# Optimization experiments

Measured on AMD Instinct MI355X. Metric: run time of the kernel, lower is better.

Reference implementation:

```python
import jax, jax.numpy as jnp
import numpy as np

N, L, V, H = 64, 2048, 32000, 512

def setup_inputs() -> dict:
    key = jax.random.key(0)
    ks = jax.random.split(key, 6)
    s = 1.0 / np.sqrt(H)
    return {
        "X": jax.random.randint(ks[0], (N, L), 0, V),
        "emb": jax.random.normal(ks[1], (V, H), jnp.float32),
        "W_hh": jax.random.normal(ks[2], (H, H), jnp.float32) * s,
        "b_hh": jax.random.normal(ks[3], (H,), jnp.float32) * s,
        "W_xh": jax.random.normal(ks[4], (H, H), jnp.float32) * s,
        "b_xh": jax.random.normal(ks[5], (H,), jnp.float32) * s,
    }

def reference(X, emb, W_hh, b_hh, W_xh, b_xh):
    # Embed all timesteps and apply the input projection once (batched GEMM);
    # identical math to per-step W_xh(E_t) + b_xh.
    E = emb[X]                                   # (N, L, H)
    Xh = jnp.einsum('nlh,kh->nlk', E, W_xh) + b_xh  # (N, L, H)

    def step(h, xh_t):
        # h_t = tanh(W_hh h_{t-1} + b_hh + W_xh x_t + b_xh)
        h = jnp.tanh(h @ W_hh.T + b_hh + xh_t)
        return h, h

    h0 = jnp.zeros((X.shape[0], W_hh.shape[0]), dtype=emb.dtype)
    _, H_all = jax.lax.scan(step, h0, jnp.swapaxes(Xh, 0, 1))  # (L, N, H)
    return jnp.swapaxes(H_all, 0, 1)             # (N, L, H)
```

## Files before the change

### kernel.cpp

```cpp
#include <hip/hip_runtime.h>


typedef _Float16 half8 __attribute__((ext_vector_type(8)));
typedef float    f32x4 __attribute__((ext_vector_type(4)));

#define MFMA_F16(A,B,C) __builtin_amdgcn_mfma_f32_16x16x32_f16(A,B,C,0,0,0)

static __device__ __forceinline__ half8 cvt8(const float* p){
  const f32x4* q = (const f32x4*)p;
  f32x4 a = q[0], b = q[1];
  half8 r;
  r[0]=(_Float16)a[0]; r[1]=(_Float16)a[1]; r[2]=(_Float16)a[2]; r[3]=(_Float16)a[3];
  r[4]=(_Float16)b[0]; r[5]=(_Float16)b[1]; r[6]=(_Float16)b[2]; r[7]=(_Float16)b[3];
  return r;
}

static __device__ __forceinline__ float tanh_fast(float z){
  float e = __expf(2.0f*z);
  return 1.0f - 2.0f/(e + 1.0f);
}

__global__ __launch_bounds__(256) void k_xh(
    const int* __restrict__ X, const float* __restrict__ emb,
    const float* __restrict__ Wxh, const float* __restrict__ bxh,
    const float* __restrict__ bhh, float* __restrict__ out)
{
  const int bid = blockIdx.x;
  const int bm = bid >> 3;
  const int bn = bid & 7;
  const int tid = threadIdx.x;
  const int w  = tid >> 6;
  const int l  = tid & 63;
  const int lr = l & 15, lq = l >> 4;

  const int mbase = bm*64 + (w>>1)*32;
  const int nbase = bn*64 + (w&1)*32;

  const int tok0 = X[mbase + lr];
  const int tok1 = X[mbase + 16 + lr];
  const int c0 = nbase + lr;
  const int c1 = nbase + 16 + lr;
  const float bs0 = bxh[c0] + bhh[c0];
  const float bs1 = bxh[c1] + bhh[c1];

  const float* a0 = emb + (long long)tok0*512 + lq*8;
  const float* a1 = emb + (long long)tok1*512 + lq*8;
  const float* b0 = Wxh + (long long)c0*512 + lq*8;
  const float* b1 = Wxh + (long long)c1*512 + lq*8;

  f32x4 acc00 = {0,0,0,0}, acc01 = {0,0,0,0}, acc10 = {0,0,0,0}, acc11 = {0,0,0,0};

  #pragma unroll
  for (int ks=0; ks<16; ++ks){
    half8 A0 = cvt8(a0 + ks*32);
    half8 A1 = cvt8(a1 + ks*32);
    half8 B0 = cvt8(b0 + ks*32);
    half8 B1 = cvt8(b1 + ks*32);
    acc00 = MFMA_F16(A0, B0, acc00);
    acc01 = MFMA_F16(A0, B1, acc01);
    acc10 = MFMA_F16(A1, B0, acc10);
    acc11 = MFMA_F16(A1, B1, acc11);
  }
  #pragma unroll
  for (int r=0; r<4; ++r){
    const long long m0 = mbase + 4*lq + r;
    const long long m1 = m0 + 16;
    out[m0*512 + c0] = acc00[r] + bs0;
    out[m0*512 + c1] = acc01[r] + bs1;
    out[m1*512 + c0] = acc10[r] + bs0;
    out[m1*512 + c1] = acc11[r] + bs1;
  }
}

__global__ __launch_bounds__(512, 2) void k_rnn(
    const float* __restrict__ Whh,
    float* __restrict__ out)
{
  const int b   = blockIdx.x;
  const int tid = threadIdx.x;
  const int w   = tid >> 6;
  const int l   = tid & 63;
  const int lr  = l & 15;
  const int kg  = l >> 4;
  const int wc0 = w * 64;

  __shared__ _Float16 wlds[8][16][512];
  __shared__ _Float16 hbuf[2][2][520];

  for (int i = tid; i < 2*2*520; i += 512) (&hbuf[0][0][0])[i] = (_Float16)0.0f;

  half8 Wv[3][16];
  #pragma unroll
  for (int ct = 0; ct < 3; ++ct){
    #pragma unroll
    for (int ks = 0; ks < 16; ++ks){
      Wv[ct][ks] = cvt8(Whh + (long long)(wc0 + ct*16 + lr)*512 + ks*32 + kg*8);
    }
  }
  #pragma unroll
  for (int ks = 0; ks < 16; ++ks){
    half8 v = cvt8(Whh + (long long)(wc0 + 48 + lr)*512 + ks*32 + kg*8);
    *(half8*)&wlds[w][ks][l*8] = v;
  }
  __syncthreads();

  const int jj = l & 1;
  const long long nb = (long long)(b*2 + (lr < 2 ? lr : 0)) * 2048 * 512;

  for (int t = 0; t < 2048; ++t){
    const int bufc = t & 1, bufp = bufc ^ 1;

    f32x4 xh0 = {0,0,0,0}, xh1 = {0,0,0,0}, xh2 = {0,0,0,0}, xh3 = {0,0,0,0};
    long long ob = 0;
    const bool act = (lr < 2);
    if (act){
      ob = nb + (long long)t*512 + wc0 + kg*4;
      xh0 = *(const f32x4*)(out + ob);
      xh1 = *(const f32x4*)(out + ob + 16);
      xh2 = *(const f32x4*)(out + ob + 32);
      xh3 = *(const f32x4*)(out + ob + 48);
    }

    f32x4 acc0 = {0,0,0,0}, acc1 = {0,0,0,0}, acc2 = {0,0,0,0}, acc3 = {0,0,0,0};

    #pragma unroll
    for (int ks = 0; ks < 16; ++ks){
      half8 hf = *(const half8*)&hbuf[bufp][jj][ks*32 + kg*8];
      half8 w3 = *(const half8*)&wlds[w][ks][l*8];
      acc0 = MFMA_F16(Wv[0][ks], hf, acc0);
      acc1 = MFMA_F16(Wv[1][ks], hf, acc1);
      acc2 = MFMA_F16(Wv[2][ks], hf, acc2);
      acc3 = MFMA_F16(w3, hf, acc3);
    }

    if (act){
      f32x4 h0, h1, h2, h3;
      #pragma unroll
      for (int r = 0; r < 4; ++r){
        h0[r] = tanh_fast(acc0[r] + xh0[r]);
        h1[r] = tanh_fast(acc1[r] + xh1[r]);
        h2[r] = tanh_fast(acc2[r] + xh2[r]);
        h3[r] = tanh_fast(acc3[r] + xh3[r]);
      }
      *(f32x4*)(out + ob)      = h0;
      *(f32x4*)(out + ob + 16) = h1;
      *(f32x4*)(out + ob + 32) = h2;
      *(f32x4*)(out + ob + 48) = h3;

      union { _Float16 h[4]; unsigned long long u; } p0, p1, p2, p3;
      #pragma unroll
      for (int r = 0; r < 4; ++r){
        p0.h[r] = (_Float16)h0[r]; p1.h[r] = (_Float16)h1[r];
        p2.h[r] = (_Float16)h2[r]; p3.h[r] = (_Float16)h3[r];
      }
      const int cl = wc0 + kg*4;
      *(unsigned long long*)&hbuf[bufc][lr][cl]      = p0.u;
      *(unsigned long long*)&hbuf[bufc][lr][cl + 16] = p1.u;
      *(unsigned long long*)&hbuf[bufc][lr][cl + 32] = p2.u;
      *(unsigned long long*)&hbuf[bufc][lr][cl + 48] = p3.u;
    }

    __syncthreads();
  }
}

extern "C" void kernel_launch(void* const* d_in, const int* in_sizes, int n_in,
                              void* d_out, int out_size, void* d_ws, size_t ws_size,
                              hipStream_t stream)
{
  const int*   X    = (const int*)  d_in[0];
  const float* emb  = (const float*)d_in[1];
  const float* Whh  = (const float*)d_in[2];
  const float* bhh  = (const float*)d_in[3];
  const float* Wxh  = (const float*)d_in[4];
  const float* bxh  = (const float*)d_in[5];
  float* out = (float*)d_out;

  hipLaunchKernelGGL(k_xh,  dim3(16384), dim3(256), 0, stream, X, emb, Wxh, bxh, bhh, out);
  hipLaunchKernelGGL(k_rnn, dim3(32),    dim3(512), 0, stream, Whh, out);
}
```

Before: 8.702 ms.

## Batch 16 sequences per RNN block with 4 waves and swizzled LDS hidden state

The recurrent kernel changes from 32 blocks of 8 waves, each handling 2 sequences padded into a 16-wide MFMA tile, to 4 blocks of 4 waves, each handling 16 sequences. That fills the MFMA N dimension instead of wasting most of it on padding. Each wave now owns 128 output columns, with W_hh split between registers (3/4) and LDS (1/4). The hidden state sits in a single XOR-swizzled LDS buffer guarded by two barriers per step instead of double buffering. The trade-off is only 4 CUs in use, more serial MFMA work per wave per timestep, and an extra barrier on the serial chain.

```diff
diff --git a/kernel.cpp b/kernel.cpp
--- a/kernel.cpp
+++ b/kernel.cpp
@@ -72,94 +72,85 @@
   }
 }
 
-__global__ __launch_bounds__(512, 2) void k_rnn(
+__global__ __launch_bounds__(256, 1) void k_rnn(
     const float* __restrict__ Whh,
     float* __restrict__ out)
 {
-  const int b   = blockIdx.x;
+  const int g   = blockIdx.x;
   const int tid = threadIdx.x;
   const int w   = tid >> 6;
   const int l   = tid & 63;
   const int lr  = l & 15;
   const int kg  = l >> 4;
-  const int wc0 = w * 64;
+  const int r7  = lr & 7;
+  const int colbase = w * 128;
 
-  __shared__ _Float16 wlds[8][16][512];
-  __shared__ _Float16 hbuf[2][2][520];
+  __shared__ _Float16 wlds[4][32][512];
+  __shared__ _Float16 hb[16][512];
 
-  for (int i = tid; i < 2*2*520; i += 512) (&hbuf[0][0][0])[i] = (_Float16)0.0f;
+  {
+    f32x4 z = {0,0,0,0};
+    f32x4* hz = (f32x4*)&hb[0][0];
+    for (int i = tid; i < 16*512*2/16; i += 256) hz[i] = z;
+  }
 
-  half8 Wv[3][16];
+  half8 Wreg[8][12];
   #pragma unroll
-  for (int ct = 0; ct < 3; ++ct){
+  for (int ct = 0; ct < 8; ++ct){
+    const float* wp = Whh + (long long)(colbase + ct*16 + lr)*512 + kg*8;
     #pragma unroll
     for (int ks = 0; ks < 16; ++ks){
-      Wv[ct][ks] = cvt8(Whh + (long long)(wc0 + ct*16 + lr)*512 + ks*32 + kg*8);
+      half8 v = cvt8(wp + ks*32);
+      if ((ks & 3) == 0) *(half8*)&wlds[w][ct*4 + (ks>>2)][l*8] = v;
+      else               Wreg[ct][ks - (ks>>2) - 1] = v;
     }
-  }
-  #pragma unroll
-  for (int ks = 0; ks < 16; ++ks){
-    half8 v = cvt8(Whh + (long long)(wc0 + 48 + lr)*512 + ks*32 + kg*8);
-    *(half8*)&wlds[w][ks][l*8] = v;
   }
   __syncthreads();
 
-  const int jj = l & 1;
-  const long long nb = (long long)(b*2 + (lr < 2 ? lr : 0)) * 2048 * 512;
+  const long long nbase = (long long)(g*16 + lr) * (2048LL*512);
 
   for (int t = 0; t < 2048; ++t){
-    const int bufc = t & 1, bufp = bufc ^ 1;
+    const float* op = out + nbase + (long long)t*512 + colbase + kg*4;
+    f32x4 xh[8];
+    #pragma unroll
+    for (int ct = 0; ct < 8; ++ct) xh[ct] = *(const f32x4*)(op + ct*16);
 
-    f32x4 xh0 = {0,0,0,0}, xh1 = {0,0,0,0}, xh2 = {0,0,0,0}, xh3 = {0,0,0,0};
-    long long ob = 0;
-    const bool act = (lr < 2);
-    if (act){
-      ob = nb + (long long)t*512 + wc0 + kg*4;
-      xh0 = *(const f32x4*)(out + ob);
-      xh1 = *(const f32x4*)(out + ob + 16);
-      xh2 = *(const f32x4*)(out + ob + 32);
-      xh3 = *(const f32x4*)(out + ob + 48);
-    }
-
-    f32x4 acc0 = {0,0,0,0}, acc1 = {0,0,0,0}, acc2 = {0,0,0,0}, acc3 = {0,0,0,0};
+    f32x4 acc[8];
+    #pragma unroll
+    for (int ct = 0; ct < 8; ++ct) acc[ct] = (f32x4){0,0,0,0};
 
     #pragma unroll
     for (int ks = 0; ks < 16; ++ks){
-      half8 hf = *(const half8*)&hbuf[bufp][jj][ks*32 + kg*8];
-      half8 w3 = *(const half8*)&wlds[w][ks][l*8];
-      acc0 = MFMA_F16(Wv[0][ks], hf, acc0);
-      acc1 = MFMA_F16(Wv[1][ks], hf, acc1);
-      acc2 = MFMA_F16(Wv[2][ks], hf, acc2);
-      acc3 = MFMA_F16(w3, hf, acc3);
+      half8 hf = *(const half8*)((const char*)&hb[lr][0] + (((4*ks + kg) ^ r7) << 4));
+      if ((ks & 3) == 0){
+        const int fs = ks >> 2;
+        #pragma unroll
+        for (int ct = 0; ct < 8; ++ct)
+          acc[ct] = MFMA_F16(*(const half8*)&wlds[w][ct*4 + fs][l*8], hf, acc[ct]);
+      } else {
+        const int j = ks - (ks>>2) - 1;
+        #pragma unroll
+        for (int ct = 0; ct < 8; ++ct)
+          acc[ct] = MFMA_F16(Wreg[ct][j], hf, acc[ct]);
+      }
     }
+    __syncthreads();
 
-    if (act){
-      f32x4 h0, h1, h2, h3;
+    #pragma unroll
+    for (int ct = 0; ct < 8; ++ct){
+      f32x4 hv;
       #pragma unroll
-      for (int r = 0; r < 4; ++r){
-        h0[r] = tanh_fast(acc0[r] + xh0[r]);
-        h1[r] = tanh_fast(acc1[r] + xh1[r]);
-        h2[r] = tanh_fast(acc2[r] + xh2[r]);
-        h3[r] = tanh_fast(acc3[r] + xh3[r]);
-      }
-      *(f32x4*)(out + ob)      = h0;
-      *(f32x4*)(out + ob + 16) = h1;
-      *(f32x4*)(out + ob + 32) = h2;
-      *(f32x4*)(out + ob + 48) = h3;
+      for (int r = 0; r < 4; ++r) hv[r] = tanh_fast(acc[ct][r] + xh[ct][r]);
+      *(f32x4*)(out + nbase + (long long)t*512 + colbase + ct*16 + kg*4) = hv;
 
-      union { _Float16 h[4]; unsigned long long u; } p0, p1, p2, p3;
+      union { _Float16 h[4]; unsigned long long u; } pk;
       #pragma unroll
-      for (int r = 0; r < 4; ++r){
-        p0.h[r] = (_Float16)h0[r]; p1.h[r] = (_Float16)h1[r];
-        p2.h[r] = (_Float16)h2[r]; p3.h[r] = (_Float16)h3[r];
-      }
-      const int cl = wc0 + kg*4;
-      *(unsigned long long*)&hbuf[bufc][lr][cl]      = p0.u;
-      *(unsigned long long*)&hbuf[bufc][lr][cl + 16] = p1.u;
-      *(unsigned long long*)&hbuf[bufc][lr][cl + 32] = p2.u;
-      *(unsigned long long*)&hbuf[bufc][lr][cl + 48] = p3.u;
+      for (int r = 0; r < 4; ++r) pk.h[r] = (_Float16)hv[r];
+      const int byte = (colbase + ct*16 + kg*4) * 2;
+      const int c0   = byte >> 4;
+      const int off8 = byte & 15;
+      *(unsigned long long*)((char*)&hb[lr][0] + (((c0 ^ r7) << 4) + off8)) = pk.u;
     }
-
     __syncthreads();
   }
 }
@@ -177,5 +168,5 @@
   float* out = (float*)d_out;
 
   hipLaunchKernelGGL(k_xh,  dim3(16384), dim3(256), 0, stream, X, emb, Wxh, bxh, bhh, out);
-  hipLaunchKernelGGL(k_rnn, dim3(32),    dim3(512), 0, stream, Whh, out);
+  hipLaunchKernelGGL(k_rnn, dim3(4),     dim3(256), 0, stream, Whh, out);
 }
```

Result: slower. 9.969 ms (+14.6%).

## Split RNN hidden columns across 4 cooperating blocks with global mailbox sync

Applied to the files above, without the earlier changes.

Reorganizes the recurrent kernel so 16 blocks each handle 16 batch rows and a quarter of the hidden columns. Each block keeps its quarter of W_hh in registers, computes its local contribution from LDS, and reads the other three quarters of h from a global mailbox after spinning on per-block step flags. This aims to use the full 16-row MFMA tile instead of wasting most lanes on only 2 batch rows per block. The trade-off is an inter-block flag handshake every timestep, whose global-memory latency and relaxed-atomic ordering could dominate or be fragile.

```diff
diff --git a/kernel.cpp b/kernel.cpp
--- a/kernel.cpp
+++ b/kernel.cpp
@@ -72,95 +72,124 @@
   }
 }
 
-__global__ __launch_bounds__(512, 2) void k_rnn(
+__global__ __launch_bounds__(256, 1) void k_rnn(
     const float* __restrict__ Whh,
-    float* __restrict__ out)
+    float* __restrict__ out,
+    unsigned long long* __restrict__ mbox,
+    unsigned int* __restrict__ flags)
 {
   const int b   = blockIdx.x;
+  const int g   = b & 3;
+  const int s   = b >> 2;
   const int tid = threadIdx.x;
   const int w   = tid >> 6;
   const int l   = tid & 63;
   const int lr  = l & 15;
   const int kg  = l >> 4;
-  const int wc0 = w * 64;
-
-  __shared__ _Float16 wlds[8][16][512];
-  __shared__ _Float16 hbuf[2][2][520];
-
-  for (int i = tid; i < 2*2*520; i += 512) (&hbuf[0][0][0])[i] = (_Float16)0.0f;
-
-  half8 Wv[3][16];
-  #pragma unroll
-  for (int ct = 0; ct < 3; ++ct){
+
+  const int wcol = s*128 + w*32;
+
+  __shared__ _Float16 hb[2][16][128];
+
+  half8 W0[16], W1[16];
+  {
+    const float* p0 = Whh + (long long)(wcol      + lr)*512 + kg*8;
+    const float* p1 = Whh + (long long)(wcol + 16 + lr)*512 + kg*8;
     #pragma unroll
     for (int ks = 0; ks < 16; ++ks){
-      Wv[ct][ks] = cvt8(Whh + (long long)(wc0 + ct*16 + lr)*512 + ks*32 + kg*8);
-    }
-  }
-  #pragma unroll
-  for (int ks = 0; ks < 16; ++ks){
-    half8 v = cvt8(Whh + (long long)(wc0 + 48 + lr)*512 + ks*32 + kg*8);
-    *(half8*)&wlds[w][ks][l*8] = v;
-  }
-  __syncthreads();
-
-  const int jj = l & 1;
-  const long long nb = (long long)(b*2 + (lr < 2 ? lr : 0)) * 2048 * 512;
+      W0[ks] = cvt8(p0 + ks*32);
+      W1[ks] = cvt8(p1 + ks*32);
+    }
+  }
+
+  const int ps0 = (s+1)&3, ps1 = (s+2)&3, ps2 = (s+3)&3;
+  const int pb0 = g + 4*ps0, pb1 = g + 4*ps1, pb2 = g + 4*ps2;
+  const int myp = (l==0) ? pb0 : (l==1) ? pb1 : pb2;
+
+  unsigned long long* mb_me = mbox + (long long)b*1024;
+
+  const long long nbase = (long long)(g*16 + lr) * (2048LL*512);
 
   for (int t = 0; t < 2048; ++t){
     const int bufc = t & 1, bufp = bufc ^ 1;
 
-    f32x4 xh0 = {0,0,0,0}, xh1 = {0,0,0,0}, xh2 = {0,0,0,0}, xh3 = {0,0,0,0};
-    long long ob = 0;
-    const bool act = (lr < 2);
-    if (act){
-      ob = nb + (long long)t*512 + wc0 + kg*4;
-      xh0 = *(const f32x4*)(out + ob);
-      xh1 = *(const f32x4*)(out + ob + 16);
-      xh2 = *(const f32x4*)(out + ob + 32);
-      xh3 = *(const f32x4*)(out + ob + 48);
-    }
-
-    f32x4 acc0 = {0,0,0,0}, acc1 = {0,0,0,0}, acc2 = {0,0,0,0}, acc3 = {0,0,0,0};
-
+    const float* op = out + nbase + (long long)t*512 + wcol + kg*4;
+    f32x4 xh0 = *(const f32x4*)(op);
+    f32x4 xh1 = *(const f32x4*)(op + 16);
+
+    f32x4 acc0 = {0,0,0,0}, acc1 = {0,0,0,0};
+
+    if (t > 0){
+      {
+        const unsigned tgt = (unsigned)t;
+        int spin = 0; int done;
+        do {
+          unsigned v = tgt;
+          if (l < 3) v = __hip_atomic_load(&flags[myp], __ATOMIC_RELAXED, __HIP_MEMORY_SCOPE_AGENT);
+          done = __all((int)(v >= tgt));
+        } while (!done && ++spin < (1<<20));
+      }
+
+      const char* hbase = (const char*)&hb[bufp][lr][0];
+      #pragma unroll
+      for (int ksl = 0; ksl < 4; ++ksl){
+        const int chunk = (4*ksl + kg) ^ (lr & 7);
+        half8 hf = *(const half8*)(hbase + (chunk << 4));
+        acc0 = MFMA_F16(W0[4*s + ksl], hf, acc0);
+        acc1 = MFMA_F16(W1[4*s + ksl], hf, acc1);
+      }
+
+      #pragma unroll
+      for (int pi = 0; pi < 3; ++pi){
+        const int ps = (pi==0) ? ps0 : (pi==1) ? ps1 : ps2;
+        const int pb = (pi==0) ? pb0 : (pi==1) ? pb1 : pb2;
+        const unsigned long long* mp = mbox + (long long)pb*1024 + bufp*512 + lr*32;
+        #pragma unroll
+        for (int ksl = 0; ksl < 4; ++ksl){
+          const int ui = 8*ksl + 2*kg;
+          unsigned long long u0 = __hip_atomic_load(&mp[ui],   __ATOMIC_RELAXED, __HIP_MEMORY_SCOPE_AGENT);
+          unsigned long long u1 = __hip_atomic_load(&mp[ui+1], __ATOMIC_RELAXED, __HIP_MEMORY_SCOPE_AGENT);
+          union { unsigned long long u[2]; half8 v; } cv;
+          cv.u[0] = u0; cv.u[1] = u1;
+          acc0 = MFMA_F16(W0[4*ps + ksl], cv.v, acc0);
+          acc1 = MFMA_F16(W1[4*ps + ksl], cv.v, acc1);
+        }
+      }
+    }
+
+    f32x4 h0, h1;
     #pragma unroll
-    for (int ks = 0; ks < 16; ++ks){
-      half8 hf = *(const half8*)&hbuf[bufp][jj][ks*32 + kg*8];
-      half8 w3 = *(const half8*)&wlds[w][ks][l*8];
-      acc0 = MFMA_F16(Wv[0][ks], hf, acc0);
-      acc1 = MFMA_F16(Wv[1][ks], hf, acc1);
-      acc2 = MFMA_F16(Wv[2][ks], hf, acc2);
-      acc3 = MFMA_F16(w3, hf, acc3);
-    }
-
-    if (act){
-      f32x4 h0, h1, h2, h3;
-      #pragma unroll
-      for (int r = 0; r < 4; ++r){
-        h0[r] = tanh_fast(acc0[r] + xh0[r]);
-        h1[r] = tanh_fast(acc1[r] + xh1[r]);
-        h2[r] = tanh_fast(acc2[r] + xh2[r]);
-        h3[r] = tanh_fast(acc3[r] + xh3[r]);
-      }
-      *(f32x4*)(out + ob)      = h0;
-      *(f32x4*)(out + ob + 16) = h1;
-      *(f32x4*)(out + ob + 32) = h2;
-      *(f32x4*)(out + ob + 48) = h3;
-
-      union { _Float16 h[4]; unsigned long long u; } p0, p1, p2, p3;
-      #pragma unroll
-      for (int r = 0; r < 4; ++r){
-        p0.h[r] = (_Float16)h0[r]; p1.h[r] = (_Float16)h1[r];
-        p2.h[r] = (_Float16)h2[r]; p3.h[r] = (_Float16)h3[r];
-      }
-      const int cl = wc0 + kg*4;
-      *(unsigned long long*)&hbuf[bufc][lr][cl]      = p0.u;
-      *(unsigned long long*)&hbuf[bufc][lr][cl + 16] = p1.u;
-      *(unsigned long long*)&hbuf[bufc][lr][cl + 32] = p2.u;
-      *(unsigned long long*)&hbuf[bufc][lr][cl + 48] = p3.u;
-    }
-
+    for (int r = 0; r < 4; ++r){
+      h0[r] = tanh_fast(acc0[r] + xh0[r]);
+      h1[r] = tanh_fast(acc1[r] + xh1[r]);
+    }
+    union { _Float16 h[4]; unsigned long long u; } p0, p1;
+    #pragma unroll
+    for (int r = 0; r < 4; ++r){ p0.h[r] = (_Float16)h0[r]; p1.h[r] = (_Float16)h1[r]; }
+
+    {
+      char* wb = (char*)&hb[bufc][lr][0];
+      const int byte0 = 64*w + 8*kg;
+      const int byte1 = byte0 + 32;
+      const int c0 = byte0 >> 4, o0 = byte0 & 15;
+      const int c1 = byte1 >> 4, o1 = byte1 & 15;
+      *(unsigned long long*)(wb + (((c0 ^ (lr&7)) << 4) + o0)) = p0.u;
+      *(unsigned long long*)(wb + (((c1 ^ (lr&7)) << 4) + o1)) = p1.u;
+    }
+    {
+      unsigned long long* mm = mb_me + bufc*512 + lr*32;
+      const int ui = 8*w + kg;
+      __hip_atomic_store(&mm[ui],     p0.u, __ATOMIC_RELAXED, __HIP_MEMORY_SCOPE_AGENT);
+      __hip_atomic_store(&mm[ui + 4], p1.u, __ATOMIC_RELAXED, __HIP_MEMORY_SCOPE_AGENT);
+    }
+
+    asm volatile("s_waitcnt vmcnt(0)" ::: "memory");
     __syncthreads();
+    if (tid == 0)
+      __hip_atomic_store(&flags[b], (unsigned)(t+1), __ATOMIC_RELAXED, __HIP_MEMORY_SCOPE_AGENT);
+
+    *(f32x4*)(op)      = h0;
+    *(f32x4*)(op + 16) = h1;
   }
 }
 
@@ -176,6 +205,10 @@
   const float* bxh  = (const float*)d_in[5];
   float* out = (float*)d_out;
 
+  unsigned long long* mbox  = (unsigned long long*)d_ws;
+  unsigned int*       flags = (unsigned int*)((char*)d_ws + 131072);
+
+  hipMemsetAsync(flags, 0, 16*sizeof(unsigned int), stream);
   hipLaunchKernelGGL(k_xh,  dim3(16384), dim3(256), 0, stream, X, emb, Wxh, bxh, bhh, out);
-  hipLaunchKernelGGL(k_rnn, dim3(32),    dim3(512), 0, stream, Whh, out);
-}
+  hipLaunchKernelGGL(k_rnn, dim3(16),    dim3(256), 0, stream, Whh, out, mbox, flags);
+}
```

Result: slower. 18.93 ms (+117.5%).
